# Performance work log

Hardware: AMD Instinct MI355X
Metric: run time of the kernel (lower is better)

## Reference

```python
import jax, jax.numpy as jnp
import numpy as np

# Static problem sizes (batch 'batch' vector is built as B equal-sized graphs).
B, N_PER, K = 4, 4096, 64          # graphs, points per graph, max_num_neighbors
RATIO, R = 0.25, 0.2               # fps ratio, radius
M = int(N_PER * RATIO)             # fps samples per graph (1024)
C_IN = 64                          # input feature channels
MLP_DIMS = [C_IN + 3, 64, 64, 128]


def setup_inputs() -> dict:
    key = jax.random.key(0)
    ks = jax.random.split(key, 8)
    x = jax.random.normal(ks[0], (B * N_PER, C_IN), dtype=jnp.float32)
    pos = jax.random.uniform(ks[1], (B * N_PER, 3), dtype=jnp.float32)
    batch = jnp.repeat(jnp.arange(B, dtype=jnp.int32), N_PER)

    def lin(k, fan_in, fan_out):
        s = 1.0 / np.sqrt(fan_in)
        return jax.random.uniform(k, (fan_in, fan_out), jnp.float32, -s, s)

    W1 = lin(ks[2], MLP_DIMS[0], MLP_DIMS[1]); b1 = jnp.zeros((MLP_DIMS[1],), jnp.float32)
    W2 = lin(ks[3], MLP_DIMS[1], MLP_DIMS[2]); b2 = jnp.zeros((MLP_DIMS[2],), jnp.float32)
    W3 = lin(ks[4], MLP_DIMS[2], MLP_DIMS[3]); b3 = jnp.zeros((MLP_DIMS[3],), jnp.float32)
    return {"x": x, "pos": pos, "batch": batch,
            "W1": W1, "b1": b1, "W2": W2, "b2": b2, "W3": W3, "b3": b3}


def _fps(pos_b):
    """Farthest point sampling on one graph. pos_b: [n,3] -> [M] int32 indices.
    Deterministic start at index 0 (PyG uses a random start)."""
    n = pos_b.shape[0]

    def step(carry, _):
        dists, last = carry
        d = jnp.sum((pos_b - pos_b[last]) ** 2, axis=-1)
        dists = jnp.minimum(dists, d)
        nxt = jnp.argmax(dists).astype(jnp.int32)
        return (dists, nxt), nxt

    init = (jnp.full((n,), jnp.inf, dtype=pos_b.dtype), jnp.int32(0))
    _, rest = jax.lax.scan(step, init, None, length=M - 1)
    return jnp.concatenate([jnp.zeros((1,), jnp.int32), rest])


def _radius(pos_b):
    """Radius neighbor search (self-query). Returns nbr [n,K] indices and valid [n,K] mask.
    Takes the K nearest in-ball neighbors (self always included, d=0)."""
    d2 = jnp.sum((pos_b[:, None, :] - pos_b[None, :, :]) ** 2, axis=-1)  # [n,n]
    neg = jnp.where(d2 <= R * R, -d2, -jnp.inf)
    vals, nbr = jax.lax.top_k(neg, K)
    return nbr, vals > -jnp.inf


def _pointconv(x_b, pos_b, nbr, valid, W1, b1, W2, b2, W3, b3):
    """PointConv: out_i = max_{j in N(i)} MLP(concat(x_j, pos_j - pos_i))."""
    rel = pos_b[nbr] - pos_b[:, None, :]                 # [n,K,3]
    feat = jnp.concatenate([x_b[nbr], rel], axis=-1)     # [n,K,C_IN+3]
    h = jax.nn.relu(feat @ W1 + b1)
    h = jax.nn.relu(h @ W2 + b2)
    h = jax.nn.relu(h @ W3 + b3)                          # [n,K,128]
    h = jnp.where(valid[..., None], h, -jnp.inf)          # mask padded neighbor slots
    return h.max(axis=1)                                  # [n,128]; self-edge guarantees validity


def reference(x, pos, batch, W1, b1, W2, b2, W3, b3):
    xb = x.reshape(B, N_PER, C_IN)
    pb = pos.reshape(B, N_PER, 3)
    nbr, valid = jax.vmap(_radius)(pb)                    # [B,n,K]
    out = jax.vmap(_pointconv, in_axes=(0, 0, 0, 0) + (None,) * 6)(
        xb, pb, nbr, valid, W1, b1, W2, b2, W3, b3)       # [B,n,128]
    idx = jax.vmap(_fps)(pb)                              # [B,M]
    x_s = jnp.take_along_axis(out, idx[..., None], axis=1).reshape(B * M, -1)
    pos_s = jnp.take_along_axis(pb, idx[..., None], axis=1).reshape(B * M, 3)
    batch_s = jnp.repeat(jnp.arange(B, dtype=batch.dtype), M)
    return x_s, pos_s, batch_s
```

## Files before the change

### kernel.cpp

```cpp
#include <hip/hip_runtime.h>

#define NPER 4096
#define MS   1024
#define CIN  64
#define LCAP 384

typedef float  f32x4 __attribute__((ext_vector_type(4)));
typedef short  s16x8 __attribute__((ext_vector_type(8)));

__device__ __forceinline__ float d2_exact(float ax, float ay, float az,
                                          float bx, float by, float bz) {
  float dx = __fsub_rn(ax, bx);
  float dy = __fsub_rn(ay, by);
  float dz = __fsub_rn(az, bz);
  return __fadd_rn(__fadd_rn(__fmul_rn(dx, dx), __fmul_rn(dy, dy)), __fmul_rn(dz, dz));
}

__device__ __forceinline__ unsigned short f2bf(float f) {
  unsigned b = __float_as_uint(f);
  return (unsigned short)((b + 0x7FFFu + ((b >> 16) & 1u)) >> 16);
}

template <int CTRL, int RMASK>
__device__ __forceinline__ unsigned long long dpp_max_step(unsigned long long k) {
  int hi = (int)(unsigned)(k >> 32);
  int lo = (int)(unsigned)(k & 0xFFFFFFFFull);
  int thi = __builtin_amdgcn_update_dpp(hi, hi, CTRL, RMASK, 0xF, false);
  int tlo = __builtin_amdgcn_update_dpp(lo, lo, CTRL, RMASK, 0xF, false);
  unsigned long long t =
      ((unsigned long long)(unsigned)thi << 32) | (unsigned)tlo;
  return t > k ? t : k;
}

__device__ __forceinline__ unsigned long long u64max(unsigned long long a,
                                                    unsigned long long b) {
  return a > b ? a : b;
}

__global__ __launch_bounds__(256) void fps_kernel(const float* __restrict__ pos,
                                                  int* __restrict__ idx_out) {
  const int b = blockIdx.x;
  const int t = threadIdx.x;
  __shared__ float4 s_pos4[NPER];
  __shared__ __align__(16) unsigned long long s_red[2][4];
  const float* pb = pos + (size_t)b * NPER * 3;
  for (int i = t; i < NPER; i += 256)
    s_pos4[i] = make_float4(pb[i * 3], pb[i * 3 + 1], pb[i * 3 + 2], 0.f);
  if (t == 0) idx_out[b * MS] = 0;
  __syncthreads();

  float px[16], py[16], pz[16], dist[16];
#pragma unroll
  for (int j = 0; j < 16; ++j) {
    float4 p = s_pos4[t + j * 256];
    px[j] = p.x; py[j] = p.y; pz[j] = p.z;
    dist[j] = __builtin_inff();
  }
  const int w = t >> 6;
  const int lane = t & 63;

  float lx = s_pos4[0].x, ly = s_pos4[0].y, lz = s_pos4[0].z;

  for (int m = 1; m < MS; ++m) {
    float bd = -1.0f;
    int bi = 0;
#pragma unroll
    for (int j = 0; j < 16; ++j) {
      float d2 = d2_exact(px[j], py[j], pz[j], lx, ly, lz);
      float nd = fminf(dist[j], d2);
      dist[j] = nd;
      if (nd > bd) { bd = nd; bi = t + j * 256; }
    }
    unsigned long long k =
        ((unsigned long long)__float_as_uint(bd) << 32) | (unsigned)(~bi);
    k = dpp_max_step<0x111, 0xF>(k);
    k = dpp_max_step<0x112, 0xF>(k);
    k = dpp_max_step<0x114, 0xF>(k);
    k = dpp_max_step<0x118, 0xF>(k);
    k = dpp_max_step<0x142, 0xA>(k);
    k = dpp_max_step<0x143, 0xC>(k);
    const int par = m & 1;
    if (lane == 63) s_red[par][w] = k;
    __syncthreads();
    ulonglong2 ab = *reinterpret_cast<const ulonglong2*>(&s_red[par][0]);
    ulonglong2 cd = *reinterpret_cast<const ulonglong2*>(&s_red[par][2]);
    unsigned long long kb = u64max(u64max(ab.x, ab.y), u64max(cd.x, cd.y));
    const int nx = (int)(~(unsigned)(kb & 0xFFFFFFFFull));
    if (t == 0) idx_out[b * MS + m] = nx;
    float4 wp = s_pos4[nx];
    lx = wp.x; ly = wp.y; lz = wp.z;
  }
}

__global__ __launch_bounds__(512, 4) void radconv_kernel(
    const float* __restrict__ x, const float* __restrict__ pos,
    const int* __restrict__ idx,
    const float* __restrict__ W1, const float* __restrict__ B1,
    const float* __restrict__ W2, const float* __restrict__ B2,
    const float* __restrict__ W3, const float* __restrict__ B3,
    float* __restrict__ out) {
  const int t = threadIdx.x;
  const int g = blockIdx.x >> 9;
  const int qpair = blockIdx.x & 511;
  const float* pb = pos + (size_t)g * NPER * 3;
  const float* xb = x + (size_t)g * NPER * CIN;

  __shared__ int s_cnt[2];
  __shared__ float s_ctr[2][4];
  __shared__ __align__(16) unsigned long long s_list[2][LCAP];
  __shared__ int s_nbr[2][64];
  __shared__ __align__(16) unsigned short sFeat[2][64 * 104];
  __shared__ __align__(16) unsigned short sW1[64 * 104];
  __shared__ __align__(16) unsigned short sW2[64 * 72];
  __shared__ __align__(16) unsigned short sW3[128 * 72];

  if (t < 2) s_cnt[t] = 0;
  const int q0 = g * MS + qpair * 2;
  const int qiA = idx[q0], qiB = idx[q0 + 1];
  const float cAx = pb[qiA * 3], cAy = pb[qiA * 3 + 1], cAz = pb[qiA * 3 + 2];
  const float cBx = pb[qiB * 3], cBy = pb[qiB * 3 + 1], cBz = pb[qiB * 3 + 2];
  if (t == 0) { s_ctr[0][0] = cAx; s_ctr[0][1] = cAy; s_ctr[0][2] = cAz; }
  if (t == 1) { s_ctr[1][0] = cBx; s_ctr[1][1] = cBy; s_ctr[1][2] = cBz; }
  __syncthreads();

  {
    float pp[24];
    const float4* pv = (const float4*)(pb + (size_t)t * 24);
#pragma unroll
    for (int r = 0; r < 6; ++r) {
      float4 v = pv[r];
      pp[r * 4 + 0] = v.x; pp[r * 4 + 1] = v.y;
      pp[r * 4 + 2] = v.z; pp[r * 4 + 3] = v.w;
    }
#pragma unroll
    for (int jj = 0; jj < 8; ++jj) {
      const int j = t * 8 + jj;
      const float X = pp[jj * 3], Y = pp[jj * 3 + 1], Z = pp[jj * 3 + 2];
      float dA = d2_exact(X, Y, Z, cAx, cAy, cAz);
      if (dA <= 0.04f) {
        int p = atomicAdd(&s_cnt[0], 1);
        if (p < LCAP)
          s_list[0][p] = ((unsigned long long)__float_as_uint(dA) << 32) | (unsigned)j;
      }
      float dB = d2_exact(X, Y, Z, cBx, cBy, cBz);
      if (dB <= 0.04f) {
        int p = atomicAdd(&s_cnt[1], 1);
        if (p < LCAP)
          s_list[1][p] = ((unsigned long long)__float_as_uint(dB) << 32) | (unsigned)j;
      }
    }
  }
  for (int ee = t; ee < 64 * 64; ee += 512) {
    int c = ee >> 6, kk = 67 + (ee & 63);
    if (kk < 104) sW1[c * 104 + kk] = 0;
  }
  for (int e = t; e < 67 * 64; e += 512) {
    int k = e >> 6, c = e & 63;
    sW1[c * 104 + k] = f2bf(W1[e]);
  }
  for (int e = t; e < 64 * 64; e += 512) {
    int k = e >> 6, c = e & 63;
    sW2[c * 72 + k] = f2bf(W2[e]);
  }
  for (int e = t; e < 64 * 128; e += 512) {
    int k = e >> 7, c = e & 127;
    sW3[c * 72 + k] = f2bf(W3[e]);
  }
  __syncthreads();

  const int w = t >> 6, lane = t & 63;
  const int c0 = min(min(s_cnt[0], LCAP), 64);
  const int c1 = min(min(s_cnt[1], LCAP), 64);

  {
    const int rq = w >> 2;
    const int nsurv = min(s_cnt[rq], LCAP);
    for (int e = (w & 3) * 64 + lane; e < nsurv; e += 256) {
      unsigned long long mykey = s_list[rq][e];
      int rank = 0;
      int o = 0;
      for (; o + 8 <= nsurv; o += 8) {
        unsigned long long k0 = s_list[rq][o + 0], k1 = s_list[rq][o + 1];
        unsigned long long k2 = s_list[rq][o + 2], k3 = s_list[rq][o + 3];
        unsigned long long k4 = s_list[rq][o + 4], k5 = s_list[rq][o + 5];
        unsigned long long k6 = s_list[rq][o + 6], k7 = s_list[rq][o + 7];
        rank += (k0 < mykey) + (k1 < mykey) + (k2 < mykey) + (k3 < mykey) +
                (k4 < mykey) + (k5 < mykey) + (k6 < mykey) + (k7 < mykey);
      }
      for (; o < nsurv; ++o) rank += (s_list[rq][o] < mykey) ? 1 : 0;
      if (rank < 64) s_nbr[rq][rank] = (int)(mykey & 0xFFFFFFFFull);
    }
  }
  __syncthreads();

  {
    const int slot = t >> 2, part = t & 3;
    const int gq = slot >> 6, s = slot & 63;
    const int cq = gq ? c1 : c0;
    unsigned short* frow = &sFeat[gq][s * 104];
    uint4 z; z.x = z.y = z.z = z.w = 0u;
    if (s < cq) {
      const int j = s_nbr[gq][s];
      const float4* xr = (const float4*)(xb + (size_t)j * CIN + part * 16);
      float4 v0 = xr[0], v1 = xr[1], v2 = xr[2], v3 = xr[3];
      uint4 w0, w1;
      w0.x = f2bf(v0.x) | ((unsigned)f2bf(v0.y) << 16);
      w0.y = f2bf(v0.z) | ((unsigned)f2bf(v0.w) << 16);
      w0.z = f2bf(v1.x) | ((unsigned)f2bf(v1.y) << 16);
      w0.w = f2bf(v1.z) | ((unsigned)f2bf(v1.w) << 16);
      w1.x = f2bf(v2.x) | ((unsigned)f2bf(v2.y) << 16);
      w1.y = f2bf(v2.z) | ((unsigned)f2bf(v2.w) << 16);
      w1.z = f2bf(v3.x) | ((unsigned)f2bf(v3.y) << 16);
      w1.w = f2bf(v3.z) | ((unsigned)f2bf(v3.w) << 16);
      *(uint4*)(frow + part * 16) = w0;
      *(uint4*)(frow + part * 16 + 8) = w1;
      uint4 rz = z;
      if (part == 0) {
        const float cx = gq ? cBx : cAx, cy = gq ? cBy : cAy, cz = gq ? cBz : cAz;
        rz.x = f2bf(pb[j * 3] - cx) | ((unsigned)f2bf(pb[j * 3 + 1] - cy) << 16);
        rz.y = (unsigned)f2bf(pb[j * 3 + 2] - cz);
      }
      *(uint4*)(frow + 64 + part * 8) = rz;
    } else {
      *(uint4*)(frow + part * 16) = z;
      *(uint4*)(frow + part * 16 + 8) = z;
      *(uint4*)(frow + 64 + part * 8) = z;
    }
  }
  __syncthreads();

  const int qq2 = w >> 2;
  const int mt = w & 3;
  const int lo = lane & 15, hi = lane >> 4;
  unsigned short* F = &sFeat[qq2][0];
  const int arow = (16 * mt + lo) * 104;
  const int hrow = (16 * mt + hi * 4) * 104;

  {
    f32x4 acc[4];
#pragma unroll
    for (int n = 0; n < 4; ++n) {
      float bb = B1[n * 16 + lo];
      acc[n] = (f32x4){bb, bb, bb, bb};
    }
    s16x8 a0 = *(const s16x8*)(F + arow + 0 + hi * 8);
    s16x8 a1 = *(const s16x8*)(F + arow + 32 + hi * 8);
    s16x8 a2 = *(const s16x8*)(F + arow + 64 + hi * 8);
#pragma unroll
    for (int n = 0; n < 4; ++n) {
      const unsigned short* Bp = &sW1[(n * 16 + lo) * 104 + hi * 8];
      s16x8 b0 = *(const s16x8*)(Bp);
      s16x8 b1 = *(const s16x8*)(Bp + 32);
      s16x8 b2 = *(const s16x8*)(Bp + 64);
      acc[n] = __builtin_amdgcn_mfma_f32_16x16x32_bf16(a0, b0, acc[n], 0, 0, 0);
      acc[n] = __builtin_amdgcn_mfma_f32_16x16x32_bf16(a1, b1, acc[n], 0, 0, 0);
      acc[n] = __builtin_amdgcn_mfma_f32_16x16x32_bf16(a2, b2, acc[n], 0, 0, 0);
    }
#pragma unroll
    for (int n = 0; n < 4; ++n)
#pragma unroll
      for (int r = 0; r < 4; ++r)
        F[hrow + r * 104 + n * 16 + lo] = f2bf(fmaxf(acc[n][r], 0.f));
  }
  {
    f32x4 acc[4];
#pragma unroll
    for (int n = 0; n < 4; ++n) {
      float bb = B2[n * 16 + lo];
      acc[n] = (f32x4){bb, bb, bb, bb};
    }
    s16x8 a0 = *(const s16x8*)(F + arow + 0 + hi * 8);
    s16x8 a1 = *(const s16x8*)(F + arow + 32 + hi * 8);
#pragma unroll
    for (int n = 0; n < 4; ++n) {
      const unsigned short* Bp = &sW2[(n * 16 + lo) * 72 + hi * 8];
      s16x8 b0 = *(const s16x8*)(Bp);
      s16x8 b1 = *(const s16x8*)(Bp + 32);
      acc[n] = __builtin_amdgcn_mfma_f32_16x16x32_bf16(a0, b0, acc[n], 0, 0, 0);
      acc[n] = __builtin_amdgcn_mfma_f32_16x16x32_bf16(a1, b1, acc[n], 0, 0, 0);
    }
#pragma unroll
    for (int n = 0; n < 4; ++n)
#pragma unroll
      for (int r = 0; r < 4; ++r)
        F[hrow + r * 104 + n * 16 + lo] = f2bf(fmaxf(acc[n][r], 0.f));
  }
  float pm[8];
  {
    const int cq = qq2 ? c1 : c0;
    f32x4 acc[8];
#pragma unroll
    for (int n = 0; n < 8; ++n) {
      float bb = B3[n * 16 + lo];
      acc[n] = (f32x4){bb, bb, bb, bb};
    }
    s16x8 a0 = *(const s16x8*)(F + arow + 0 + hi * 8);
    s16x8 a1 = *(const s16x8*)(F + arow + 32 + hi * 8);
#pragma unroll
    for (int n = 0; n < 8; ++n) {
      const unsigned short* Bp = &sW3[(n * 16 + lo) * 72 + hi * 8];
      s16x8 b0 = *(const s16x8*)(Bp);
      s16x8 b1 = *(const s16x8*)(Bp + 32);
      acc[n] = __builtin_amdgcn_mfma_f32_16x16x32_bf16(a0, b0, acc[n], 0, 0, 0);
      acc[n] = __builtin_amdgcn_mfma_f32_16x16x32_bf16(a1, b1, acc[n], 0, 0, 0);
    }
#pragma unroll
    for (int n = 0; n < 8; ++n) {
      float v = -1e30f;
#pragma unroll
      for (int r = 0; r < 4; ++r) {
        int row = 16 * mt + hi * 4 + r;
        if (row < cq) v = fmaxf(v, fmaxf(acc[n][r], 0.f));
      }
      pm[n] = v;
    }
  }
  __syncthreads();

  float* red = (float*)&sFeat[0][0];
#pragma unroll
  for (int n = 0; n < 8; ++n)
    red[((qq2 * 128) + n * 16 + lo) * 17 + mt * 4 + hi] = pm[n];
  __syncthreads();

  if (t < 256) {
    const int gq = t >> 7, cc = t & 127;
    const float* rp = red + (gq * 128 + cc) * 17;
    float v = rp[0];
#pragma unroll
    for (int p = 1; p < 16; ++p) v = fmaxf(v, rp[p]);
    out[(size_t)(q0 + gq) * 128 + cc] = v;
  }
  if (t == 256 || t == 257) {
    const int gq = t - 256;
    const int qrow = q0 + gq;
    out[524288 + qrow * 3 + 0] = s_ctr[gq][0];
    out[524288 + qrow * 3 + 1] = s_ctr[gq][1];
    out[524288 + qrow * 3 + 2] = s_ctr[gq][2];
    out[536576 + qrow] = (float)g;
  }
}

extern "C" void kernel_launch(void* const* d_in, const int* in_sizes, int n_in,
                              void* d_out, int out_size, void* d_ws, size_t ws_size,
                              hipStream_t stream) {
  const float* x   = (const float*)d_in[0];
  const float* pos = (const float*)d_in[1];
  const float* W1  = (const float*)d_in[3];
  const float* B1  = (const float*)d_in[4];
  const float* W2  = (const float*)d_in[5];
  const float* B2  = (const float*)d_in[6];
  const float* W3  = (const float*)d_in[7];
  const float* B3  = (const float*)d_in[8];
  float* out = (float*)d_out;
  int* idx = (int*)d_ws;

  fps_kernel<<<4, 256, 0, stream>>>(pos, idx);
  radconv_kernel<<<2048, 512, 0, stream>>>(x, pos, idx, W1, B1, W2, B2, W3, B3, out);
}
```

Before: 652.1 us.

## Process two graphs per FPS block to interleave independent sampling chains

Result: slower. 1.145 ms (+75.6%).

```diff
diff --git a/kernel.cpp b/kernel.cpp
--- a/kernel.cpp
+++ b/kernel.cpp
@@ -37,58 +37,102 @@
   return a > b ? a : b;
 }
 
-__global__ __launch_bounds__(256) void fps_kernel(const float* __restrict__ pos,
-                                                  int* __restrict__ idx_out) {
-  const int b = blockIdx.x;
+__device__ __forceinline__ unsigned long long wave_max_key(unsigned long long k) {
+  k = dpp_max_step<0x111, 0xF>(k);
+  k = dpp_max_step<0x112, 0xF>(k);
+  k = dpp_max_step<0x114, 0xF>(k);
+  k = dpp_max_step<0x118, 0xF>(k);
+  k = dpp_max_step<0x142, 0xA>(k);
+  k = dpp_max_step<0x143, 0xC>(k);
+  return k;
+}
+
+__global__ __launch_bounds__(256) void fps_kernel2(const float* __restrict__ pos,
+                                                   int* __restrict__ idx_out) {
+  const int b0 = blockIdx.x * 2;
   const int t = threadIdx.x;
-  __shared__ float4 s_pos4[NPER];
-  __shared__ __align__(16) unsigned long long s_red[2][4];
-  const float* pb = pos + (size_t)b * NPER * 3;
-  for (int i = t; i < NPER; i += 256)
-    s_pos4[i] = make_float4(pb[i * 3], pb[i * 3 + 1], pb[i * 3 + 2], 0.f);
-  if (t == 0) idx_out[b * MS] = 0;
-  __syncthreads();
-
-  float px[16], py[16], pz[16], dist[16];
+  __shared__ float4 sA[NPER];
+  __shared__ float4 sB[NPER];
+  __shared__ __align__(16) unsigned long long s_redA[2][4];
+  __shared__ __align__(16) unsigned long long s_redB[2][4];
+  const float* pA = pos + (size_t)b0 * NPER * 3;
+  const float* pB = pos + (size_t)(b0 + 1) * NPER * 3;
+  for (int i = t; i < NPER; i += 256) {
+    sA[i] = make_float4(pA[i * 3], pA[i * 3 + 1], pA[i * 3 + 2], 0.f);
+    sB[i] = make_float4(pB[i * 3], pB[i * 3 + 1], pB[i * 3 + 2], 0.f);
+  }
+  if (t == 0) {
+    idx_out[b0 * MS] = 0;
+    idx_out[(b0 + 1) * MS] = 0;
+  }
+  __syncthreads();
+
+  float pxA[16], pyA[16], pzA[16], dA[16];
+  float pxB[16], pyB[16], pzB[16], dB[16];
 #pragma unroll
   for (int j = 0; j < 16; ++j) {
-    float4 p = s_pos4[t + j * 256];
-    px[j] = p.x; py[j] = p.y; pz[j] = p.z;
-    dist[j] = __builtin_inff();
+    float4 a = sA[t + j * 256];
+    pxA[j] = a.x; pyA[j] = a.y; pzA[j] = a.z;
+    dA[j] = __builtin_inff();
+    float4 c = sB[t + j * 256];
+    pxB[j] = c.x; pyB[j] = c.y; pzB[j] = c.z;
+    dB[j] = __builtin_inff();
   }
   const int w = t >> 6;
   const int lane = t & 63;
 
-  float lx = s_pos4[0].x, ly = s_pos4[0].y, lz = s_pos4[0].z;
+  float lxA = sA[0].x, lyA = sA[0].y, lzA = sA[0].z;
+  float lxB = sB[0].x, lyB = sB[0].y, lzB = sB[0].z;
 
   for (int m = 1; m < MS; ++m) {
-    float bd = -1.0f;
-    int bi = 0;
-#pragma unroll
-    for (int j = 0; j < 16; ++j) {
-      float d2 = d2_exact(px[j], py[j], pz[j], lx, ly, lz);
-      float nd = fminf(dist[j], d2);
-      dist[j] = nd;
-      if (nd > bd) { bd = nd; bi = t + j * 256; }
-    }
-    unsigned long long k =
-        ((unsigned long long)__float_as_uint(bd) << 32) | (unsigned)(~bi);
-    k = dpp_max_step<0x111, 0xF>(k);
-    k = dpp_max_step<0x112, 0xF>(k);
-    k = dpp_max_step<0x114, 0xF>(k);
-    k = dpp_max_step<0x118, 0xF>(k);
-    k = dpp_max_step<0x142, 0xA>(k);
-    k = dpp_max_step<0x143, 0xC>(k);
     const int par = m & 1;
-    if (lane == 63) s_red[par][w] = k;
+    {
+      float bd = -1.0f;
+      int bi = 0;
+#pragma unroll
+      for (int j = 0; j < 16; ++j) {
+        float d2 = d2_exact(pxA[j], pyA[j], pzA[j], lxA, lyA, lzA);
+        float nd = fminf(dA[j], d2);
+        dA[j] = nd;
+        if (nd > bd) { bd = nd; bi = t + j * 256; }
+      }
+      unsigned long long k =
+          ((unsigned long long)__float_as_uint(bd) << 32) | (unsigned)(~bi);
+      k = wave_max_key(k);
+      if (lane == 63) s_redA[par][w] = k;
+    }
+    {
+      float bd = -1.0f;
+      int bi = 0;
+#pragma unroll
+      for (int j = 0; j < 16; ++j) {
+        float d2 = d2_exact(pxB[j], pyB[j], pzB[j], lxB, lyB, lzB);
+        float nd = fminf(dB[j], d2);
+        dB[j] = nd;
+        if (nd > bd) { bd = nd; bi = t + j * 256; }
+      }
+      unsigned long long k =
+          ((unsigned long long)__float_as_uint(bd) << 32) | (unsigned)(~bi);
+      k = wave_max_key(k);
+      if (lane == 63) s_redB[par][w] = k;
+    }
     __syncthreads();
-    ulonglong2 ab = *reinterpret_cast<const ulonglong2*>(&s_red[par][0]);
-    ulonglong2 cd = *reinterpret_cast<const ulonglong2*>(&s_red[par][2]);
-    unsigned long long kb = u64max(u64max(ab.x, ab.y), u64max(cd.x, cd.y));
-    const int nx = (int)(~(unsigned)(kb & 0xFFFFFFFFull));
-    if (t == 0) idx_out[b * MS + m] = nx;
-    float4 wp = s_pos4[nx];
-    lx = wp.x; ly = wp.y; lz = wp.z;
+    ulonglong2 a0 = *reinterpret_cast<const ulonglong2*>(&s_redA[par][0]);
+    ulonglong2 a1 = *reinterpret_cast<const ulonglong2*>(&s_redA[par][2]);
+    ulonglong2 c0 = *reinterpret_cast<const ulonglong2*>(&s_redB[par][0]);
+    ulonglong2 c1 = *reinterpret_cast<const ulonglong2*>(&s_redB[par][2]);
+    unsigned long long kA = u64max(u64max(a0.x, a0.y), u64max(a1.x, a1.y));
+    unsigned long long kB = u64max(u64max(c0.x, c0.y), u64max(c1.x, c1.y));
+    const int nxA = (int)(~(unsigned)(kA & 0xFFFFFFFFull));
+    const int nxB = (int)(~(unsigned)(kB & 0xFFFFFFFFull));
+    if (t == 0) {
+      idx_out[b0 * MS + m] = nxA;
+      idx_out[(b0 + 1) * MS + m] = nxB;
+    }
+    float4 wpA = sA[nxA];
+    float4 wpB = sB[nxB];
+    lxA = wpA.x; lyA = wpA.y; lzA = wpA.z;
+    lxB = wpB.x; lyB = wpB.y; lzB = wpB.z;
   }
 }
 
@@ -355,6 +399,6 @@
   float* out = (float*)d_out;
   int* idx = (int*)d_ws;
 
-  fps_kernel<<<4, 256, 0, stream>>>(pos, idx);
+  fps_kernel2<<<2, 256, 0, stream>>>(pos, idx);
   radconv_kernel<<<2048, 512, 0, stream>>>(x, pos, idx, W1, B1, W2, B2, W3, B3, out);
 }
```
